# Performance work log

Hardware: AMD Instinct MI355X
Metric: run time of the kernel (lower is better)

The kernel has to match this reference:

```python
import jax, jax.numpy as jnp
import numpy as np

B, V, K, DIN, H, DH, OBS, HID = 2048, 3, 32, 256, 8, 64, 128, 256
REP = H * DH
EPS = 1e-6


def _ln(x, g, b):
    mu = x.mean(-1, keepdims=True)
    var = ((x - mu) ** 2).mean(-1, keepdims=True)
    return (x - mu) * jax.lax.rsqrt(var + 1e-5) * g + b


def setup_inputs() -> dict:
    key = jax.random.key(0)
    ks = iter(jax.random.split(key, 32))
    nrm = lambda shape, s=0.05: jax.random.normal(next(ks), shape, jnp.float32) * s
    return {
        'x_anchor': jax.random.normal(next(ks), (B, V, DIN), jnp.float32),
        'x_neighbors': jax.random.normal(next(ks), (B, V, K, DIN), jnp.float32),
        'edge_weights': jax.random.uniform(next(ks), (B, V, K), jnp.float32),
        'g': jax.random.normal(next(ks), (B, OBS), jnp.float32),
        'aW': nrm((V, DIN, REP)), 'ab': jnp.zeros((V, REP)), 'ag': jnp.ones((V, REP)), 'abeta': jnp.zeros((V, REP)),
        'nW': nrm((V, DIN, REP)), 'nb': jnp.zeros((V, REP)), 'ng': jnp.ones((V, REP)), 'nbeta': jnp.zeros((V, REP)),
        'Wq': nrm((V, H, DH, DH)), 'Wk': nrm((V, H, DH, DH)), 'Wv': nrm((V, H, DH, DH)), 'Wo': nrm((V, H, DH, DH)),
        'geom_log_scale': jnp.zeros((V, H)),
        'cWq': nrm((H, DH, DH)), 'cWk': nrm((H, DH, DH)), 'cWv': nrm((H, DH, DH)), 'cWo': nrm((H, DH, DH)),
        'rW1': nrm((OBS, HID)), 'rb1': jnp.zeros((HID,)),
        'rW2': nrm((HID, HID)), 'rb2': jnp.zeros((HID,)),
        'vW': nrm((HID, H * V)), 'vb': jnp.zeros((H * V,)),
        'mW': nrm((HID, H)), 'mb': jnp.zeros((H,)),
        'gW': nrm((HID, H)), 'gb': jnp.zeros((H,)),
    }


def reference(x_anchor, x_neighbors, edge_weights, g, aW, ab, ag, abeta, nW, nb, ng, nbeta,
              Wq, Wk, Wv, Wo, geom_log_scale, cWq, cWk, cWv, cWo,
              rW1, rb1, rW2, rb2, vW, vb, mW, mb, gW, gb):
    # --- per-view encoders (vectorized over V with a leading v axis) ---
    ha = _ln(jnp.einsum('bvi,vio->bvo', x_anchor, aW) + ab, ag, abeta).reshape(B, V, H, DH)
    hn = _ln(jnp.einsum('bvki,vio->bvko', x_neighbors, nW) + nb[:, None, :],
             ng[:, None, :], nbeta[:, None, :]).reshape(B, V, K, H, DH)
    q = jnp.einsum('bvhd,vhde->bvhe', ha, Wq)
    k = jnp.einsum('bvkhd,vhde->bvkhe', hn, Wk)
    vv = jnp.einsum('bvkhd,vhde->bvkhe', hn, Wv)
    sc = jnp.einsum('bvhd,bvkhd->bvhk', q, k) / np.sqrt(DH).astype(np.float32)
    geom = jax.nn.softplus(geom_log_scale)  # [V,H]
    sc = sc + geom[None, :, :, None] * jnp.log(edge_weights[:, :, None, :] + EPS)
    attn = jax.nn.softmax(sc, axis=-1)
    ho = jnp.einsum('bvhk,bvkhd->bvhd', attn, vv)
    ho = jnp.einsum('bvhd,vhde->bvhe', ho, Wo) + ha  # residual
    view_tokens = jnp.transpose(ho, (0, 2, 1, 3))  # [B,H,V,Dh]
    # --- router ---
    hid = jax.nn.gelu(jnp.dot(g, rW1) + rb1, approximate=False)
    hid = jax.nn.gelu(jnp.dot(hid, rW2) + rb2, approximate=False)
    pi = jax.nn.softmax((jnp.dot(hid, vW) + vb).reshape(B, H, V), axis=-1)
    beta = jax.nn.sigmoid((jnp.dot(hid, mW) + mb)[..., None])  # [B,H,1]
    gate = jax.nn.softmax(jnp.dot(hid, gW) + gb, axis=-1)      # [B,H]
    # --- pi-weighted mixture + cross-view interaction with log-pi prior ---
    mix = jnp.einsum('bhv,bhvd->bhd', pi, view_tokens)
    qc = jnp.einsum('bhd,hde->bhe', mix, cWq)
    kc = jnp.einsum('bhvd,hde->bhve', view_tokens, cWk)
    vc = jnp.einsum('bhvd,hde->bhve', view_tokens, cWv)
    s2 = jnp.einsum('bhd,bhvd->bhv', qc, kc) / np.sqrt(DH).astype(np.float32) + jnp.log(pi + EPS)
    a2 = jax.nn.softmax(s2, axis=-1)
    cr = jnp.einsum('bhv,bhvd->bhd', a2, vc)
    cr = jnp.einsum('bhd,hde->bhe', cr, cWo)
    # mode blend + head gating; head_repr kept unflattened [B,H,Dh]
    return gate[..., None] * (beta * cr + (1.0 - beta) * mix)
```

## Files before the change

kernel.cpp:

```cpp
#include <hip/hip_runtime.h>

#define B_   2048
#define V_   3
#define K_   32
#define DIN_ 256
#define H_   8
#define DH_  64
#define REP_ 512

typedef unsigned short u16;
typedef unsigned int   u32;
typedef __bf16 bf8 __attribute__((ext_vector_type(8)));
typedef float  f4  __attribute__((ext_vector_type(4)));

static __device__ __forceinline__ u16 f2bf(float f) {
  union { float f; u32 i; } x; x.f = f;
  u32 r = (x.i + 0x7FFFu + ((x.i >> 16) & 1u)) >> 16;
  return (u16)r;
}
static __device__ __forceinline__ float bflo(u32 q) {
  union { u32 i; float f; } x; x.i = q << 16; return x.f;
}
static __device__ __forceinline__ float bfhi(u32 q) {
  union { u32 i; float f; } x; x.i = q & 0xffff0000u; return x.f;
}
static __device__ __forceinline__ u32 pk2bf(float lo, float hi) {
  u32 r;
  asm("v_cvt_pk_bf16_f32 %0, %1, %2" : "=v"(r) : "v"(lo), "v"(hi));
  return r;
}

__global__ __launch_bounds__(256) void k0_fuse(
    const float* __restrict__ nW, const float* __restrict__ aW,
    const float* __restrict__ Wv,
    const float* __restrict__ Wq, const float* __restrict__ Wk,
    u16* __restrict__ nWt, u16* __restrict__ aWt, u16* __restrict__ Wvt,
    float* __restrict__ Wqk)
{
  __shared__ float sm8[8192];
  int bid = blockIdx.x, t = threadIdx.x;
  if (bid < 1536) {
    int id = bid * 256 + t;
    int v  = id / 131072, r  = id % 131072;
    int kt = r / 16384,   r2 = r % 16384;
    int n  = r2 >> 5;
    int s  = (r2 >> 3) & 3;
    int m  = r2 & 7;
    int c  = s ^ ((n >> 1) & 3);
    int k  = kt * 32 + c * 8 + m;
    int src = (v * 256 + k) * 512 + n;
    nWt[id] = f2bf(nW[src]);
    aWt[id] = f2bf(aW[src]);
  } else if (bid < 1920) {
    int j = (bid - 1536) * 256 + t;
    int vh = j >> 12, r = j & 4095;
    int e = r >> 6, d = r & 63;
    Wvt[j] = f2bf(Wv[(vh * 64 + d) * 64 + e]);
  } else {
    int vh = bid - 1920;
    float* wq = sm8;
    float* wkT = sm8 + 4096;
    #pragma unroll
    for (int i = 0; i < 16; ++i) {
      int idx = i * 256 + t;
      wq[idx] = Wq[(long)vh * 4096 + idx];
      int e = idx >> 6, c = idx & 63;
      wkT[c * 64 + e] = Wk[(long)vh * 4096 + e * 64 + c];
    }
    __syncthreads();
    int d = t >> 2, e0 = (t & 3) * 16;
    float acc[16];
    #pragma unroll
    for (int j = 0; j < 16; ++j) acc[j] = 0.f;
    for (int c = 0; c < 64; ++c) {
      float a = wq[d * 64 + c];
      const float* wr = &wkT[c * 64 + e0];
      #pragma unroll
      for (int j = 0; j < 16; ++j) acc[j] += a * wr[j];
    }
    #pragma unroll
    for (int j = 0; j < 16; ++j) Wqk[(long)vh * 4096 + d * 64 + e0 + j] = acc[j];
  }
}

__global__ __launch_bounds__(256) void k_tq(
    const float* __restrict__ ha, const float* __restrict__ Wqk,
    float* __restrict__ tB)
{
  __shared__ float hs[512];
  int bv = blockIdx.x, t = threadIdx.x;
  int v = bv % 3;
  hs[t]       = ha[(long)bv * 512 + t];
  hs[256 + t] = ha[(long)bv * 512 + 256 + t];
  __syncthreads();
  int h = t >> 5, e0 = (t & 31) * 2;
  const float* wq = Wqk + ((long)v * 8 + h) * 4096 + e0;
  const float* hv = &hs[h * 64];
  float a0 = 0.f, a1 = 0.f;
  #pragma unroll 4
  for (int d = 0; d < 64; ++d) {
    float x = hv[d];
    float2 wv = *(const float2*)&wq[d * 64];
    a0 += x * wv.x;
    a1 += x * wv.y;
  }
  tB[(long)bv * 512 + h * 64 + e0]     = a0 * 0.125f;
  tB[(long)bv * 512 + h * 64 + e0 + 1] = a1 * 0.125f;
}

__global__ __launch_bounds__(512, 4) void k1a_anchor(
    const float* __restrict__ X,
    const u16*   __restrict__ Wt,
    const float* __restrict__ bias,
    const float* __restrict__ gamma,
    const float* __restrict__ betap,
    float* __restrict__ ha)
{
  __shared__ u16 A[64 * 256];
  __shared__ u16 Bt[16384];
  __shared__ float lnP1[256], lnP2[256], muRs[128];

  const int v = blockIdx.y, blk = blockIdx.x, t = threadIdx.x;
  const int w = t >> 6, l = t & 63, lm = l & 15, lg = l >> 4;
  const int wm = w & 1, wn = w >> 1;

  const u16* Wbase = Wt + (long)v * 131072;

  uint4 pf[4];
  {
    const uint4* gp = (const uint4*)(Wbase + t * 8);
    #pragma unroll
    for (int r = 0; r < 4; ++r) pf[r] = gp[r * 512];
  }

  {
    int row = t >> 3;
    int cbase = (t & 7) * 32;
    int b = blk * 64 + row;
    const float4* src = (const float4*)(X + (long)(b * 3 + v) * 256 + cbase);
    int sw = row & 7;
    #pragma unroll
    for (int j = 0; j < 8; ++j) {
      float4 f = src[j];
      int col = cbase + j * 4;
      int c = col >> 3, m = col & 7;
      uint2 u;
      u.x = pk2bf(f.x, f.y);
      u.y = pk2bf(f.z, f.w);
      *(uint2*)&A[row * 256 + ((c ^ sw) << 3) + m] = u;
    }
  }

  f4 acc[2][8];
  #pragma unroll
  for (int i = 0; i < 2; ++i)
    #pragma unroll
    for (int j = 0; j < 8; ++j) { f4 z = {0.f, 0.f, 0.f, 0.f}; acc[i][j] = z; }

  for (int kt = 0; kt < 8; ++kt) {
    __syncthreads();
    *(uint4*)&Bt[t * 8]         = pf[0];
    *(uint4*)&Bt[t * 8 + 4096]  = pf[1];
    *(uint4*)&Bt[t * 8 + 8192]  = pf[2];
    *(uint4*)&Bt[t * 8 + 12288] = pf[3];
    __syncthreads();
    if (kt < 7) {
      const uint4* gp = (const uint4*)(Wbase + (kt + 1) * 16384 + t * 8);
      #pragma unroll
      for (int r = 0; r < 4; ++r) pf[r] = gp[r * 512];
    }
    bf8 af[2];
    #pragma unroll
    for (int tm = 0; tm < 2; ++tm) {
      int row = wm * 32 + tm * 16 + lm;
      int c = kt * 4 + lg;
      af[tm] = *(const bf8*)&A[row * 256 + ((c ^ (row & 7)) << 3)];
    }
    #pragma unroll
    for (int tn = 0; tn < 8; ++tn) {
      int n = wn * 128 + tn * 16 + lm;
      bf8 bv = *(const bf8*)&Bt[n * 32 + ((lg ^ ((n >> 1) & 3)) << 3)];
      acc[0][tn] = __builtin_amdgcn_mfma_f32_16x16x32_bf16(bv, af[0], acc[0][tn], 0, 0, 0);
      acc[1][tn] = __builtin_amdgcn_mfma_f32_16x16x32_bf16(bv, af[1], acc[1][tn], 0, 0, 0);
    }
  }

  #pragma unroll
  for (int tn = 0; tn < 8; ++tn) {
    float4 bb = *(const float4*)&bias[v * 512 + wn * 128 + tn * 16 + lg * 4];
    #pragma unroll
    for (int r = 0; r < 4; ++r) { acc[0][tn][r] += ((const float*)&bb)[r]; acc[1][tn][r] += ((const float*)&bb)[r]; }
  }

  #pragma unroll
  for (int tm = 0; tm < 2; ++tm) {
    float s1 = 0.f, s2 = 0.f;
    #pragma unroll
    for (int tn = 0; tn < 8; ++tn)
      #pragma unroll
      for (int r = 0; r < 4; ++r) { float z = acc[tm][tn][r]; s1 += z; s2 += z * z; }
    s1 += __shfl_xor(s1, 16, 64); s2 += __shfl_xor(s2, 16, 64);
    s1 += __shfl_xor(s1, 32, 64); s2 += __shfl_xor(s2, 32, 64);
    if (lg == 0) {
      int row = wm * 32 + tm * 16 + lm;
      lnP1[row * 4 + wn] = s1;
      lnP2[row * 4 + wn] = s2;
    }
  }
  __syncthreads();
  if (t < 64) {
    float p = lnP1[t * 4] + lnP1[t * 4 + 1] + lnP1[t * 4 + 2] + lnP1[t * 4 + 3];
    float q = lnP2[t * 4] + lnP2[t * 4 + 1] + lnP2[t * 4 + 2] + lnP2[t * 4 + 3];
    float mu = p * (1.f / 512.f);
    float var = q * (1.f / 512.f) - mu * mu;
    muRs[t]      = mu;
    muRs[64 + t] = rsqrtf(var + 1e-5f);
  }
  __syncthreads();

  {
    float mu0 = muRs[wm * 32 + lm],      rs0 = muRs[64 + wm * 32 + lm];
    float mu1 = muRs[wm * 32 + 16 + lm], rs1 = muRs[64 + wm * 32 + 16 + lm];
    int b0g = blk * 64 + wm * 32 + lm, b1g = b0g + 16;
    #pragma unroll
    for (int tn = 0; tn < 8; ++tn) {
      int col0 = wn * 128 + tn * 16 + lg * 4;
      float4 g4 = *(const float4*)&gamma[v * 512 + col0];
      float4 b4 = *(const float4*)&betap[v * 512 + col0];
      float4 y;
      y.x = (acc[0][tn][0] - mu0) * rs0 * g4.x + b4.x;
      y.y = (acc[0][tn][1] - mu0) * rs0 * g4.y + b4.y;
      y.z = (acc[0][tn][2] - mu0) * rs0 * g4.z + b4.z;
      y.w = (acc[0][tn][3] - mu0) * rs0 * g4.w + b4.w;
      *(float4*)&ha[(long)(b0g * 3 + v) * 512 + col0] = y;
      y.x = (acc[1][tn][0] - mu1) * rs1 * g4.x + b4.x;
      y.y = (acc[1][tn][1] - mu1) * rs1 * g4.y + b4.y;
      y.z = (acc[1][tn][2] - mu1) * rs1 * g4.z + b4.z;
      y.w = (acc[1][tn][3] - mu1) * rs1 * g4.w + b4.w;
      *(float4*)&ha[(long)(b1g * 3 + v) * 512 + col0] = y;
    }
  }
}

union K12Smem {
  struct { u16 A[64 * 256]; u16 Bt[16384]; } p;
  u16 S[64 * 512];
};

__global__ __launch_bounds__(512, 4) void k12_fused(
    const float* __restrict__ X,
    const u16*   __restrict__ Wt,
    const float* __restrict__ bias,
    const float* __restrict__ gamma,
    const float* __restrict__ betap,
    const float* __restrict__ ha,
    const u16*   __restrict__ Wvt,
    const float* __restrict__ tB,
    const float* __restrict__ Wo,
    const float* __restrict__ ew,
    const float* __restrict__ gls,
    float* __restrict__ vt)
{
  __shared__ K12Smem sm;
  __shared__ float tS[1024];
  __shared__ float aS[512];
  __shared__ float oSbuf[1024];
  float* lnP1 = oSbuf;
  float* lnP2 = oSbuf + 256;
  float* muRs = oSbuf + 512;

  const int v = blockIdx.y, blk = blockIdx.x, t = threadIdx.x;
  const int w = t >> 6, l = t & 63, lm = l & 15, lg = l >> 4;
  const int wm = w & 1, wn = w >> 1;

  const u16* Wbase = Wt + (long)v * 131072;

  uint4 pf[4];
  {
    const uint4* gp = (const uint4*)(Wbase + t * 8);
    #pragma unroll
    for (int r = 0; r < 4; ++r) pf[r] = gp[r * 512];
  }

  {
    int row = t >> 3;
    int cbase = (t & 7) * 32;
    int b = blk * 2 + (row >> 5);
    long grow = ((long)(b * 3 + v) * 32 + (row & 31)) * 256;
    const float4* src = (const float4*)(X + grow + cbase);
    int sw = row & 7;
    #pragma unroll
    for (int j = 0; j < 8; ++j) {
      float4 f = src[j];
      int col = cbase + j * 4;
      int c = col >> 3, m = col & 7;
      uint2 u;
      u.x = pk2bf(f.x, f.y);
      u.y = pk2bf(f.z, f.w);
      *(uint2*)&sm.p.A[row * 256 + ((c ^ sw) << 3) + m] = u;
    }
  }
  {
    int b = t >> 8, e = (t & 255) * 2;
    *(float2*)&tS[b * 512 + e] =
        *(const float2*)&tB[((long)(blk * 2 + b) * 3 + v) * 512 + e];
  }

  f4 acc[2][8];
  #pragma unroll
  for (int i = 0; i < 2; ++i)
    #pragma unroll
    for (int j = 0; j < 8; ++j) { f4 z = {0.f, 0.f, 0.f, 0.f}; acc[i][j] = z; }

  for (int kt = 0; kt < 8; ++kt) {
    __syncthreads();
    *(uint4*)&sm.p.Bt[t * 8]         = pf[0];
    *(uint4*)&sm.p.Bt[t * 8 + 4096]  = pf[1];
    *(uint4*)&sm.p.Bt[t * 8 + 8192]  = pf[2];
    *(uint4*)&sm.p.Bt[t * 8 + 12288] = pf[3];
    __syncthreads();
    if (kt < 7) {
      const uint4* gp = (const uint4*)(Wbase + (kt + 1) * 16384 + t * 8);
      #pragma unroll
      for (int r = 0; r < 4; ++r) pf[r] = gp[r * 512];
    }
    bf8 af[2];
    #pragma unroll
    for (int tm = 0; tm < 2; ++tm) {
      int row = wm * 32 + tm * 16 + lm;
      int c = kt * 4 + lg;
      af[tm] = *(const bf8*)&sm.p.A[row * 256 + ((c ^ (row & 7)) << 3)];
    }
    #pragma unroll
    for (int tn = 0; tn < 8; ++tn) {
      int n = wn * 128 + tn * 16 + lm;
      bf8 bv = *(const bf8*)&sm.p.Bt[n * 32 + ((lg ^ ((n >> 1) & 3)) << 3)];
      acc[0][tn] = __builtin_amdgcn_mfma_f32_16x16x32_bf16(bv, af[0], acc[0][tn], 0, 0, 0);
      acc[1][tn] = __builtin_amdgcn_mfma_f32_16x16x32_bf16(bv, af[1], acc[1][tn], 0, 0, 0);
    }
  }

  #pragma unroll
  for (int tn = 0; tn < 8; ++tn) {
    float4 bb = *(const float4*)&bias[v * 512 + wn * 128 + tn * 16 + lg * 4];
    #pragma unroll
    for (int r = 0; r < 4; ++r) { acc[0][tn][r] += ((const float*)&bb)[r]; acc[1][tn][r] += ((const float*)&bb)[r]; }
  }

  #pragma unroll
  for (int tm = 0; tm < 2; ++tm) {
    float s1 = 0.f, s2 = 0.f;
    #pragma unroll
    for (int tn = 0; tn < 8; ++tn)
      #pragma unroll
      for (int r = 0; r < 4; ++r) { float z = acc[tm][tn][r]; s1 += z; s2 += z * z; }
    s1 += __shfl_xor(s1, 16, 64); s2 += __shfl_xor(s2, 16, 64);
    s1 += __shfl_xor(s1, 32, 64); s2 += __shfl_xor(s2, 32, 64);
    if (lg == 0) {
      int row = wm * 32 + tm * 16 + lm;
      lnP1[row * 4 + wn] = s1;
      lnP2[row * 4 + wn] = s2;
    }
  }
  __syncthreads();
  if (t < 64) {
    float p = lnP1[t * 4] + lnP1[t * 4 + 1] + lnP1[t * 4 + 2] + lnP1[t * 4 + 3];
    float q = lnP2[t * 4] + lnP2[t * 4 + 1] + lnP2[t * 4 + 2] + lnP2[t * 4 + 3];
    float mu = p * (1.f / 512.f);
    float var = q * (1.f / 512.f) - mu * mu;
    muRs[t]      = mu;
    muRs[64 + t] = rsqrtf(var + 1e-5f);
  }
  __syncthreads();

  {
    float mu0 = muRs[wm * 32 + lm],      rs0 = muRs[64 + wm * 32 + lm];
    float mu1 = muRs[wm * 32 + 16 + lm], rs1 = muRs[64 + wm * 32 + 16 + lm];
    int row0 = wm * 32 + lm, row1 = row0 + 16;
    int sw0 = row0 & 7, sw1 = row1 & 7;
    #pragma unroll
    for (int tn = 0; tn < 8; ++tn) {
      int col0 = wn * 128 + tn * 16 + lg * 4;
      int c = col0 >> 3, m0 = col0 & 7;
      float4 g4 = *(const float4*)&gamma[v * 512 + col0];
      float4 b4 = *(const float4*)&betap[v * 512 + col0];
      {
        float y0 = (acc[0][tn][0] - mu0) * rs0 * g4.x + b4.x;
        float y1 = (acc[0][tn][1] - mu0) * rs0 * g4.y + b4.y;
        float y2 = (acc[0][tn][2] - mu0) * rs0 * g4.z + b4.z;
        float y3 = (acc[0][tn][3] - mu0) * rs0 * g4.w + b4.w;
        uint2 p;
        p.x = pk2bf(y0, y1);
        p.y = pk2bf(y2, y3);
        *(uint2*)&sm.S[row0 * 512 + ((c ^ sw0) << 3) + m0] = p;
      }
      {
        float y0 = (acc[1][tn][0] - mu1) * rs1 * g4.x + b4.x;
        float y1 = (acc[1][tn][1] - mu1) * rs1 * g4.y + b4.y;
        float y2 = (acc[1][tn][2] - mu1) * rs1 * g4.z + b4.z;
        float y3 = (acc[1][tn][3] - mu1) * rs1 * g4.w + b4.w;
        uint2 p;
        p.x = pk2bf(y0, y1);
        p.y = pk2bf(y2, y3);
        *(uint2*)&sm.S[row1 * 512 + ((c ^ sw1) << 3) + m0] = p;
      }
    }
  }
  __syncthreads();

  {
    int b = t >> 8, h = (t >> 5) & 7, k = t & 31;
    float x = gls[v * 8 + h];
    float gsc = (x > 20.f) ? x : log1pf(expf(x));
    int r = b * 32 + k, sw = r & 7;
    const float* tb = &tS[(b * 8 + h) * 64];
    float s = 0.f;
    #pragma unroll
    for (int j = 0; j < 8; ++j) {
      int c8 = h * 8 + j;
      uint4 q = *(const uint4*)&sm.S[r * 512 + ((c8 ^ sw) << 3)];
      const float* tj = tb + j * 8;
      s += tj[0] * bflo(q.x) + tj[1] * bfhi(q.x)
         + tj[2] * bflo(q.y) + tj[3] * bfhi(q.y)
         + tj[4] * bflo(q.z) + tj[5] * bfhi(q.z)
         + tj[6] * bflo(q.w) + tj[7] * bfhi(q.w);
    }
    float e_w = ew[((long)(blk * 2 + b) * 3 + v) * 32 + k];
    s += gsc * logf(e_w + 1e-6f);
    float m = s;
    #pragma unroll
    for (int d = 1; d < 32; d <<= 1) m = fmaxf(m, __shfl_xor(m, d, 64));
    float exs = expf(s - m), sum = exs;
    #pragma unroll
    for (int d = 1; d < 32; d <<= 1) sum += __shfl_xor(sum, d, 64);
    aS[(b * 8 + h) * 32 + k] = exs / sum;
  }
  __syncthreads();

  #pragma unroll 1
  for (int i = 0; i < 2; ++i) {
    int p = w * 2 + i, b = p >> 3, h = p & 7;
    const u16* wvg = Wvt + (long)(v * 8 + h) * 4096;
    f4 aV[2][4];
    #pragma unroll
    for (int a = 0; a < 2; ++a)
      #pragma unroll
      for (int j = 0; j < 4; ++j) { f4 z = {0.f, 0.f, 0.f, 0.f}; aV[a][j] = z; }
    #pragma unroll
    for (int ks = 0; ks < 2; ++ks) {
      int ko = ks * 32 + lg * 8;
      bf8 af[2];
      #pragma unroll
      for (int tm = 0; tm < 2; ++tm) {
        int r = b * 32 + tm * 16 + lm;
        int c8 = h * 8 + ks * 4 + lg;
        af[tm] = *(const bf8*)&sm.S[r * 512 + ((c8 ^ (r & 7)) << 3)];
      }
      #pragma unroll
      for (int tn = 0; tn < 4; ++tn) {
        bf8 bv = *(const bf8*)&wvg[(tn * 16 + lm) * 64 + ko];
        #pragma unroll
        for (int tm = 0; tm < 2; ++tm)
          aV[tm][tn] = __builtin_amdgcn_mfma_f32_16x16x32_bf16(af[tm], bv, aV[tm][tn], 0, 0, 0);
      }
    }
    float pp[4] = {0.f, 0.f, 0.f, 0.f};
    #pragma unroll
    for (int tm = 0; tm < 2; ++tm)
      #pragma unroll
      for (int r4 = 0; r4 < 4; ++r4) {
        int k = tm * 16 + lg * 4 + r4;
        float a = aS[p * 32 + k];
        #pragma unroll
        for (int tn = 0; tn < 4; ++tn) pp[tn] += a * aV[tm][tn][r4];
      }
    #pragma unroll
    for (int tn = 0; tn < 4; ++tn) {
      float x = pp[tn];
      x += __shfl_xor(x, 16, 64);
      x += __shfl_xor(x, 32, 64);
      if (l < 16) oSbuf[p * 64 + tn * 16 + lm] = x;
    }
  }
  __syncthreads();

  {
    int h = t >> 6, e = t & 63;
    const float* wo = Wo + (long)(v * 8 + h) * 4096;
    float a0 = ha[((long)(blk * 2 + 0) * 3 + v) * 512 + h * 64 + e];
    float a1 = ha[((long)(blk * 2 + 1) * 3 + v) * 512 + h * 64 + e];
    const float* o0 = &oSbuf[h * 64];
    const float* o1 = &oSbuf[512 + h * 64];
    #pragma unroll 8
    for (int d = 0; d < 64; ++d) {
      float wv = wo[d * 64 + e];
      a0 += o0[d] * wv;
      a1 += o1[d] * wv;
    }
    vt[(((long)(blk * 2 + 0) * 8 + h) * 3 + v) * 64 + e] = a0;
    vt[(((long)(blk * 2 + 1) * 8 + h) * 3 + v) * 64 + e] = a1;
  }
}

__global__ __launch_bounds__(256) void k34_router_cross(
    const float* __restrict__ g,
    const float* __restrict__ rW1, const float* __restrict__ rb1,
    const float* __restrict__ rW2, const float* __restrict__ rb2,
    const float* __restrict__ vW, const float* __restrict__ vb,
    const float* __restrict__ mW, const float* __restrict__ mb,
    const float* __restrict__ gW, const float* __restrict__ gb,
    const float* __restrict__ vtg,
    const float* __restrict__ cWq, const float* __restrict__ cWk,
    const float* __restrict__ cWv, const float* __restrict__ cWo,
    float* __restrict__ out)
{
  __shared__ float smem[12544];
  __shared__ float gs[512], h1[1024], h2[1024], lgt[160];
  float* vts   = smem;
  float* mixs  = smem + 6144;
  float* buf1  = smem + 8192;
  float* buf2  = smem + 10240;
  float* a2s   = smem + 12288;
  float* pis   = smem + 12384;
  float* betas = smem + 12480;
  float* gates = smem + 12512;

  int t = threadIdx.x, bb = blockIdx.x * 4;

  {
    const float4* src = (const float4*)(vtg + (long)bb * 1536);
    #pragma unroll
    for (int r = 0; r < 6; ++r) ((float4*)vts)[r * 256 + t] = src[r * 256 + t];
    gs[t]       = g[(long)bb * 128 + t];
    gs[256 + t] = g[(long)bb * 128 + 256 + t];
  }
  __syncthreads();

  {
    int bl = t >> 6, e0 = (t & 63) * 4;
    float acc[4];
    #pragma unroll
    for (int j = 0; j < 4; ++j) acc[j] = rb1[e0 + j];
    for (int i = 0; i < 128; ++i) {
      float gv = gs[bl * 128 + i];
      const float* wr = rW1 + i * 256 + e0;
      #pragma unroll
      for (int j = 0; j < 4; ++j) acc[j] += gv * wr[j];
    }
    #pragma unroll
    for (int j = 0; j < 4; ++j) { float x = acc[j]; h1[bl * 256 + e0 + j] = 0.5f * x * (1.f + erff(x * 0.70710678118f)); }
  }
  __syncthreads();
  {
    int bl = t >> 6, e0 = (t & 63) * 4;
    float acc[4];
    #pragma unroll
    for (int j = 0; j < 4; ++j) acc[j] = rb2[e0 + j];
    for (int i = 0; i < 256; ++i) {
      float hv = h1[bl * 256 + i];
      const float* wr = rW2 + i * 256 + e0;
      #pragma unroll
      for (int j = 0; j < 4; ++j) acc[j] += hv * wr[j];
    }
    #pragma unroll
    for (int j = 0; j < 4; ++j) { float x = acc[j]; h2[bl * 256 + e0 + j] = 0.5f * x * (1.f + erff(x * 0.70710678118f)); }
  }
  __syncthreads();
  if (t < 160) {
    int bl = t / 40, j = t % 40;
    const float* W; float bs; int col, stride;
    if (j < 24)      { W = vW; col = j;      stride = 24; bs = vb[j]; }
    else if (j < 32) { W = mW; col = j - 24; stride = 8;  bs = mb[j - 24]; }
    else             { W = gW; col = j - 32; stride = 8;  bs = gb[j - 32]; }
    float acc = bs;
    for (int i = 0; i < 256; ++i) acc += h2[bl * 256 + i] * W[i * stride + col];
    lgt[bl * 40 + j] = acc;
  }
  __syncthreads();
  if (t < 4) {
    const float* L = &lgt[t * 40];
    #pragma unroll
    for (int hh = 0; hh < 8; ++hh) {
      float a0 = L[hh * 3], a1 = L[hh * 3 + 1], a2v = L[hh * 3 + 2];
      float m = fmaxf(a0, fmaxf(a1, a2v));
      float x0 = expf(a0 - m), x1 = expf(a1 - m), x2 = expf(a2v - m);
      float inv = 1.f / (x0 + x1 + x2);
      pis[t * 24 + hh * 3 + 0] = x0 * inv;
      pis[t * 24 + hh * 3 + 1] = x1 * inv;
      pis[t * 24 + hh * 3 + 2] = x2 * inv;
      betas[t * 8 + hh] = 1.f / (1.f + expf(-L[24 + hh]));
    }
    float m = L[32];
    #pragma unroll
    for (int hh = 1; hh < 8; ++hh) m = fmaxf(m, L[32 + hh]);
    float s = 0.f, ex[8];
    #pragma unroll
    for (int hh = 0; hh < 8; ++hh) { ex[hh] = expf(L[32 + hh] - m); s += ex[hh]; }
    float inv = 1.f / s;
    #pragma unroll
    for (int hh = 0; hh < 8; ++hh) gates[t * 8 + hh] = ex[hh] * inv;
  }
  __syncthreads();

  int bl = t >> 6, hh = (t >> 3) & 7, e0 = (t & 7) * 8;
  const float* vbh = &vts[(bl * 8 + hh) * 192];
  {
    float p0 = pis[bl * 24 + hh * 3], p1 = pis[bl * 24 + hh * 3 + 1], p2 = pis[bl * 24 + hh * 3 + 2];
    #pragma unroll
    for (int j = 0; j < 8; ++j) {
      int e = e0 + j;
      mixs[(bl * 8 + hh) * 64 + e] = p0 * vbh[e] + p1 * vbh[64 + e] + p2 * vbh[128 + e];
    }
  }
  __syncthreads();
  {
    float acc[8] = {0.f,0.f,0.f,0.f,0.f,0.f,0.f,0.f};
    const float* M = &mixs[(bl * 8 + hh) * 64];
    for (int d = 0; d < 64; ++d) {
      float mv = M[d];
      const float* wr = &cWq[(hh * 64 + d) * 64 + e0];
      #pragma unroll
      for (int j = 0; j < 8; ++j) acc[j] += mv * wr[j];
    }
    #pragma unroll
    for (int j = 0; j < 8; ++j) buf1[(bl * 8 + hh) * 64 + e0 + j] = acc[j] * 0.125f;
  }
  __syncthreads();
  {
    const float* Q = &buf1[(bl * 8 + hh) * 64];
    #pragma unroll
    for (int d2 = 0; d2 < 8; ++d2) {
      const float* wr = &cWk[(hh * 64 + e0 + d2) * 64];
      float a = 0.f;
      for (int e = 0; e < 64; ++e) a += wr[e] * Q[e];
      buf2[(bl * 8 + hh) * 64 + e0 + d2] = a;
    }
  }
  __syncthreads();
  if (t < 32) {
    int b2 = t >> 3, h2 = t & 7;
    const float* Wd = &buf2[(b2 * 8 + h2) * 64];
    const float* vb2 = &vts[(b2 * 8 + h2) * 192];
    float s[3];
    #pragma unroll
    for (int v3 = 0; v3 < 3; ++v3) {
      float a = 0.f;
      for (int d = 0; d < 64; ++d) a += Wd[d] * vb2[v3 * 64 + d];
      s[v3] = a + logf(pis[b2 * 24 + h2 * 3 + v3] + 1e-6f);
    }
    float m = fmaxf(s[0], fmaxf(s[1], s[2]));
    float x0 = expf(s[0] - m), x1 = expf(s[1] - m), x2 = expf(s[2] - m);
    float inv = 1.f / (x0 + x1 + x2);
    a2s[(b2 * 8 + h2) * 3 + 0] = x0 * inv;
    a2s[(b2 * 8 + h2) * 3 + 1] = x1 * inv;
    a2s[(b2 * 8 + h2) * 3 + 2] = x2 * inv;
  }
  __syncthreads();
  {
    float a0 = a2s[(bl * 8 + hh) * 3], a1 = a2s[(bl * 8 + hh) * 3 + 1], a2v = a2s[(bl * 8 + hh) * 3 + 2];
    #pragma unroll
    for (int j = 0; j < 8; ++j) {
      int e = e0 + j;
      buf1[(bl * 8 + hh) * 64 + e] = a0 * vbh[e] + a1 * vbh[64 + e] + a2v * vbh[128 + e];
    }
  }
  __syncthreads();
  {
    float acc[8] = {0.f,0.f,0.f,0.f,0.f,0.f,0.f,0.f};
    const float* Y = &buf1[(bl * 8 + hh) * 64];
    for (int d = 0; d < 64; ++d) {
      float yv = Y[d];
      const float* wr = &cWv[(hh * 64 + d) * 64 + e0];
      #pragma unroll
      for (int j = 0; j < 8; ++j) acc[j] += yv * wr[j];
    }
    #pragma unroll
    for (int j = 0; j < 8; ++j) buf2[(bl * 8 + hh) * 64 + e0 + j] = acc[j];
  }
  __syncthreads();
  {
    float acc[8] = {0.f,0.f,0.f,0.f,0.f,0.f,0.f,0.f};
    const float* C2 = &buf2[(bl * 8 + hh) * 64];
    for (int d = 0; d < 64; ++d) {
      float cv = C2[d];
      const float* wr = &cWo[(hh * 64 + d) * 64 + e0];
      #pragma unroll
      for (int j = 0; j < 8; ++j) acc[j] += cv * wr[j];
    }
    float bt = betas[bl * 8 + hh], gt = gates[bl * 8 + hh];
    const float* M = &mixs[(bl * 8 + hh) * 64];
    #pragma unroll
    for (int j = 0; j < 8; ++j)
      out[((long)(bb + bl) * 8 + hh) * 64 + e0 + j] = gt * (bt * acc[j] + (1.f - bt) * M[e0 + j]);
  }
}

extern "C" void kernel_launch(void* const* d_in, const int* in_sizes, int n_in,
                              void* d_out, int out_size, void* d_ws, size_t ws_size,
                              hipStream_t stream) {
  const float* x_anchor    = (const float*)d_in[0];
  const float* x_neighbors = (const float*)d_in[1];
  const float* edge_w      = (const float*)d_in[2];
  const float* g           = (const float*)d_in[3];
  const float* aW  = (const float*)d_in[4];
  const float* ab  = (const float*)d_in[5];
  const float* ag  = (const float*)d_in[6];
  const float* abeta = (const float*)d_in[7];
  const float* nW  = (const float*)d_in[8];
  const float* nb  = (const float*)d_in[9];
  const float* ng  = (const float*)d_in[10];
  const float* nbeta = (const float*)d_in[11];
  const float* Wq  = (const float*)d_in[12];
  const float* Wk  = (const float*)d_in[13];
  const float* Wv  = (const float*)d_in[14];
  const float* Wo  = (const float*)d_in[15];
  const float* gls = (const float*)d_in[16];
  const float* cWq = (const float*)d_in[17];
  const float* cWk = (const float*)d_in[18];
  const float* cWv = (const float*)d_in[19];
  const float* cWo = (const float*)d_in[20];
  const float* rW1 = (const float*)d_in[21];
  const float* rb1 = (const float*)d_in[22];
  const float* rW2 = (const float*)d_in[23];
  const float* rb2 = (const float*)d_in[24];
  const float* vW  = (const float*)d_in[25];
  const float* vb  = (const float*)d_in[26];
  const float* mW  = (const float*)d_in[27];
  const float* mb  = (const float*)d_in[28];
  const float* gW  = (const float*)d_in[29];
  const float* gb  = (const float*)d_in[30];

  char* p = (char*)d_ws;
  u16* nWt = (u16*)p;  p += 786432;
  u16* aWt = (u16*)p;  p += 786432;
  u16* Wvt = (u16*)p;  p += 196608;
  float* WqkB = (float*)p; p += 393216;
  float* ha   = (float*)p; p += 12582912;
  float* vtb  = (float*)p; p += 12582912;
  float* tqB  = (float*)p; p += 12582912;
  (void)ws_size;

  k0_fuse<<<1944, 256, 0, stream>>>(nW, aW, Wv, Wq, Wk, nWt, aWt, Wvt, WqkB);
  k1a_anchor<<<dim3(32, 3), 512, 0, stream>>>(x_anchor, aWt, ab, ag, abeta, ha);
  k_tq<<<6144, 256, 0, stream>>>(ha, WqkB, tqB);
  k12_fused<<<dim3(1024, 3), 512, 0, stream>>>(x_neighbors, nWt, nb, ng, nbeta,
                                               ha, Wvt, tqB, Wo, edge_w, gls, vtb);
  k34_router_cross<<<512, 256, 0, stream>>>(g, rW1, rb1, rW2, rb2, vW, vb,
                                            mW, mb, gW, gb, vtb,
                                            cWq, cWk, cWv, cWo, (float*)d_out);
}
```

Baseline: 900.4 us.

## Use direct global-to-LDS weight loads and double-buffer B in 1024-thread k12

Weight tiles are now loaded with global_load_lds straight into shared memory instead of staging through registers. In k1a the fill happens after a barrier each k-step. k12_fused gets a double-buffered B tile so the next tile's load overlaps the current MFMAs. k12 is also widened from 512 to 1024 threads, with each wave owning one 16-row M tile and one attention head, which cuts registers per thread and raises parallelism but increases LDS use per block (extra B buffer plus separate LN scratch) and may reduce resident blocks. Correctness relies on the barrier placement, and there is no explicit wait for the asynchronous LDS loads.

```diff
diff --git a/kernel.cpp b/kernel.cpp
--- a/kernel.cpp
+++ b/kernel.cpp
@@ -28,6 +28,12 @@
   u32 r;
   asm("v_cvt_pk_bf16_f32 %0, %1, %2" : "=v"(r) : "v"(lo), "v"(hi));
   return r;
+}
+
+static __device__ __forceinline__ void gl2lds16(const u16* g, u16* l) {
+  __builtin_amdgcn_global_load_lds(
+      (const __attribute__((address_space(1))) unsigned int*)(g),
+      (__attribute__((address_space(3))) unsigned int*)(l), 16, 0, 0);
 }
 
 __global__ __launch_bounds__(256) void k0_fuse(
@@ -126,11 +132,11 @@
 
   const u16* Wbase = Wt + (long)v * 131072;
 
-  uint4 pf[4];
-  {
-    const uint4* gp = (const uint4*)(Wbase + t * 8);
-    #pragma unroll
-    for (int r = 0; r < 4; ++r) pf[r] = gp[r * 512];
+  {
+    const u16* gp = Wbase + t * 8;
+    u16* lp = &Bt[t * 8];
+    #pragma unroll
+    for (int r = 0; r < 4; ++r) gl2lds16(gp + r * 4096, lp + r * 4096);
   }
 
   {
@@ -158,17 +164,14 @@
     for (int j = 0; j < 8; ++j) { f4 z = {0.f, 0.f, 0.f, 0.f}; acc[i][j] = z; }
 
   for (int kt = 0; kt < 8; ++kt) {
+    if (kt) {
+      __syncthreads();
+      const u16* gp = Wbase + kt * 16384 + t * 8;
+      u16* lp = &Bt[t * 8];
+      #pragma unroll
+      for (int r = 0; r < 4; ++r) gl2lds16(gp + r * 4096, lp + r * 4096);
+    }
     __syncthreads();
-    *(uint4*)&Bt[t * 8]         = pf[0];
-    *(uint4*)&Bt[t * 8 + 4096]  = pf[1];
-    *(uint4*)&Bt[t * 8 + 8192]  = pf[2];
-    *(uint4*)&Bt[t * 8 + 12288] = pf[3];
-    __syncthreads();
-    if (kt < 7) {
-      const uint4* gp = (const uint4*)(Wbase + (kt + 1) * 16384 + t * 8);
-      #pragma unroll
-      for (int r = 0; r < 4; ++r) pf[r] = gp[r * 512];
-    }
     bf8 af[2];
     #pragma unroll
     for (int tm = 0; tm < 2; ++tm) {
@@ -243,11 +246,11 @@
 }
 
 union K12Smem {
-  struct { u16 A[64 * 256]; u16 Bt[16384]; } p;
+  struct { u16 A[64 * 256]; u16 Bt[2][16384]; } p;
   u16 S[64 * 512];
 };
 
-__global__ __launch_bounds__(512, 4) void k12_fused(
+__global__ __launch_bounds__(1024, 4) void k12_fused(
     const float* __restrict__ X,
     const u16*   __restrict__ Wt,
     const float* __restrict__ bias,
@@ -265,34 +268,32 @@
   __shared__ float tS[1024];
   __shared__ float aS[512];
   __shared__ float oSbuf[1024];
-  float* lnP1 = oSbuf;
-  float* lnP2 = oSbuf + 256;
-  float* muRs = oSbuf + 512;
+  __shared__ float lnP1[256], lnP2[256], muRs[128];
 
   const int v = blockIdx.y, blk = blockIdx.x, t = threadIdx.x;
   const int w = t >> 6, l = t & 63, lm = l & 15, lg = l >> 4;
-  const int wm = w & 1, wn = w >> 1;
+  const int wm = w & 3, wn = w >> 2;
 
   const u16* Wbase = Wt + (long)v * 131072;
 
-  uint4 pf[4];
-  {
-    const uint4* gp = (const uint4*)(Wbase + t * 8);
-    #pragma unroll
-    for (int r = 0; r < 4; ++r) pf[r] = gp[r * 512];
-  }
-
-  {
-    int row = t >> 3;
-    int cbase = (t & 7) * 32;
+  {
+    const u16* gp = Wbase + t * 8;
+    u16* lp = &sm.p.Bt[0][t * 8];
+    gl2lds16(gp, lp);
+    gl2lds16(gp + 8192, lp + 8192);
+  }
+
+  {
+    int row = t >> 4;
+    int cq = (t & 15) * 4;
     int b = blk * 2 + (row >> 5);
     long grow = ((long)(b * 3 + v) * 32 + (row & 31)) * 256;
-    const float4* src = (const float4*)(X + grow + cbase);
+    const float* src = X + grow;
     int sw = row & 7;
     #pragma unroll
-    for (int j = 0; j < 8; ++j) {
-      float4 f = src[j];
-      int col = cbase + j * 4;
+    for (int j = 0; j < 4; ++j) {
+      int col = cq + j * 64;
+      float4 f = *(const float4*)(src + col);
       int c = col >> 3, m = col & 7;
       uint2 u;
       u.x = pk2bf(f.x, f.y);
@@ -301,42 +302,32 @@
     }
   }
   {
-    int b = t >> 8, e = (t & 255) * 2;
-    *(float2*)&tS[b * 512 + e] =
-        *(const float2*)&tB[((long)(blk * 2 + b) * 3 + v) * 512 + e];
-  }
-
-  f4 acc[2][8];
+    int b = t >> 9, e = t & 511;
+    tS[t] = tB[((long)(blk * 2 + b) * 3 + v) * 512 + e];
+  }
+
+  f4 acc[8];
   #pragma unroll
-  for (int i = 0; i < 2; ++i)
-    #pragma unroll
-    for (int j = 0; j < 8; ++j) { f4 z = {0.f, 0.f, 0.f, 0.f}; acc[i][j] = z; }
-
+  for (int j = 0; j < 8; ++j) { f4 z = {0.f, 0.f, 0.f, 0.f}; acc[j] = z; }
+
+  const int rowA = wm * 16 + lm;
+  const int swA = rowA & 7;
   for (int kt = 0; kt < 8; ++kt) {
     __syncthreads();
-    *(uint4*)&sm.p.Bt[t * 8]         = pf[0];
-    *(uint4*)&sm.p.Bt[t * 8 + 4096]  = pf[1];
-    *(uint4*)&sm.p.Bt[t * 8 + 8192]  = pf[2];
-    *(uint4*)&sm.p.Bt[t * 8 + 12288] = pf[3];
-    __syncthreads();
     if (kt < 7) {
-      const uint4* gp = (const uint4*)(Wbase + (kt + 1) * 16384 + t * 8);
-      #pragma unroll
-      for (int r = 0; r < 4; ++r) pf[r] = gp[r * 512];
-    }
-    bf8 af[2];
-    #pragma unroll
-    for (int tm = 0; tm < 2; ++tm) {
-      int row = wm * 32 + tm * 16 + lm;
-      int c = kt * 4 + lg;
-      af[tm] = *(const bf8*)&sm.p.A[row * 256 + ((c ^ (row & 7)) << 3)];
-    }
+      const u16* gp = Wbase + (kt + 1) * 16384 + t * 8;
+      u16* lp = &sm.p.Bt[(kt + 1) & 1][t * 8];
+      gl2lds16(gp, lp);
+      gl2lds16(gp + 8192, lp + 8192);
+    }
+    int c = kt * 4 + lg;
+    bf8 af = *(const bf8*)&sm.p.A[rowA * 256 + ((c ^ swA) << 3)];
+    const u16* Bcur = sm.p.Bt[kt & 1];
     #pragma unroll
     for (int tn = 0; tn < 8; ++tn) {
       int n = wn * 128 + tn * 16 + lm;
-      bf8 bv = *(const bf8*)&sm.p.Bt[n * 32 + ((lg ^ ((n >> 1) & 3)) << 3)];
-      acc[0][tn] = __builtin_amdgcn_mfma_f32_16x16x32_bf16(bv, af[0], acc[0][tn], 0, 0, 0);
-      acc[1][tn] = __builtin_amdgcn_mfma_f32_16x16x32_bf16(bv, af[1], acc[1][tn], 0, 0, 0);
+      bf8 bv = *(const bf8*)&Bcur[n * 32 + ((lg ^ ((n >> 1) & 3)) << 3)];
+      acc[tn] = __builtin_amdgcn_mfma_f32_16x16x32_bf16(bv, af, acc[tn], 0, 0, 0);
     }
   }
 
@@ -344,22 +335,20 @@
   for (int tn = 0; tn < 8; ++tn) {
     float4 bb = *(const float4*)&bias[v * 512 + wn * 128 + tn * 16 + lg * 4];
     #pragma unroll
-    for (int r = 0; r < 4; ++r) { acc[0][tn][r] += ((const float*)&bb)[r]; acc[1][tn][r] += ((const float*)&bb)[r]; }
-  }
-
-  #pragma unroll
-  for (int tm = 0; tm < 2; ++tm) {
+    for (int r = 0; r < 4; ++r) acc[tn][r] += ((const float*)&bb)[r];
+  }
+
+  {
     float s1 = 0.f, s2 = 0.f;
     #pragma unroll
     for (int tn = 0; tn < 8; ++tn)
       #pragma unroll
-      for (int r = 0; r < 4; ++r) { float z = acc[tm][tn][r]; s1 += z; s2 += z * z; }
+      for (int r = 0; r < 4; ++r) { float z = acc[tn][r]; s1 += z; s2 += z * z; }
     s1 += __shfl_xor(s1, 16, 64); s2 += __shfl_xor(s2, 16, 64);
     s1 += __shfl_xor(s1, 32, 64); s2 += __shfl_xor(s2, 32, 64);
     if (lg == 0) {
-      int row = wm * 32 + tm * 16 + lm;
-      lnP1[row * 4 + wn] = s1;
-      lnP2[row * 4 + wn] = s2;
+      lnP1[rowA * 4 + wn] = s1;
+      lnP2[rowA * 4 + wn] = s2;
     }
   }
   __syncthreads();
@@ -374,41 +363,26 @@
   __syncthreads();
 
   {
-    float mu0 = muRs[wm * 32 + lm],      rs0 = muRs[64 + wm * 32 + lm];
-    float mu1 = muRs[wm * 32 + 16 + lm], rs1 = muRs[64 + wm * 32 + 16 + lm];
-    int row0 = wm * 32 + lm, row1 = row0 + 16;
-    int sw0 = row0 & 7, sw1 = row1 & 7;
+    float mu0 = muRs[rowA], rs0 = muRs[64 + rowA];
     #pragma unroll
     for (int tn = 0; tn < 8; ++tn) {
       int col0 = wn * 128 + tn * 16 + lg * 4;
       int c = col0 >> 3, m0 = col0 & 7;
       float4 g4 = *(const float4*)&gamma[v * 512 + col0];
       float4 b4 = *(const float4*)&betap[v * 512 + col0];
-      {
-        float y0 = (acc[0][tn][0] - mu0) * rs0 * g4.x + b4.x;
-        float y1 = (acc[0][tn][1] - mu0) * rs0 * g4.y + b4.y;
-        float y2 = (acc[0][tn][2] - mu0) * rs0 * g4.z + b4.z;
-        float y3 = (acc[0][tn][3] - mu0) * rs0 * g4.w + b4.w;
-        uint2 p;
-        p.x = pk2bf(y0, y1);
-        p.y = pk2bf(y2, y3);
-        *(uint2*)&sm.S[row0 * 512 + ((c ^ sw0) << 3) + m0] = p;
-      }
-      {
-        float y0 = (acc[1][tn][0] - mu1) * rs1 * g4.x + b4.x;
-        float y1 = (acc[1][tn][1] - mu1) * rs1 * g4.y + b4.y;
-        float y2 = (acc[1][tn][2] - mu1) * rs1 * g4.z + b4.z;
-        float y3 = (acc[1][tn][3] - mu1) * rs1 * g4.w + b4.w;
-        uint2 p;
-        p.x = pk2bf(y0, y1);
-        p.y = pk2bf(y2, y3);
-        *(uint2*)&sm.S[row1 * 512 + ((c ^ sw1) << 3) + m0] = p;
-      }
-    }
-  }
-  __syncthreads();
-
-  {
+      float y0 = (acc[tn][0] - mu0) * rs0 * g4.x + b4.x;
+      float y1 = (acc[tn][1] - mu0) * rs0 * g4.y + b4.y;
+      float y2 = (acc[tn][2] - mu0) * rs0 * g4.z + b4.z;
+      float y3 = (acc[tn][3] - mu0) * rs0 * g4.w + b4.w;
+      uint2 p;
+      p.x = pk2bf(y0, y1);
+      p.y = pk2bf(y2, y3);
+      *(uint2*)&sm.S[rowA * 512 + ((c ^ swA) << 3) + m0] = p;
+    }
+  }
+  __syncthreads();
+
+  if (t < 512) {
     int b = t >> 8, h = (t >> 5) & 7, k = t & 31;
     float x = gls[v * 8 + h];
     float gsc = (x > 20.f) ? x : log1pf(expf(x));
@@ -437,10 +411,9 @@
   }
   __syncthreads();
 
-  #pragma unroll 1
-  for (int i = 0; i < 2; ++i) {
-    int p = w * 2 + i, b = p >> 3, h = p & 7;
-    const u16* wvg = Wvt + (long)(v * 8 + h) * 4096;
+  {
+    int p = w, b = w >> 3, h = w & 7;
+    const u16* wvg = Wvt + ((long)v * 8 + h) * 4096;
     f4 aV[2][4];
     #pragma unroll
     for (int a = 0; a < 2; ++a)
@@ -449,19 +422,19 @@
     #pragma unroll
     for (int ks = 0; ks < 2; ++ks) {
       int ko = ks * 32 + lg * 8;
-      bf8 af[2];
+      bf8 af2[2];
       #pragma unroll
       for (int tm = 0; tm < 2; ++tm) {
         int r = b * 32 + tm * 16 + lm;
         int c8 = h * 8 + ks * 4 + lg;
-        af[tm] = *(const bf8*)&sm.S[r * 512 + ((c8 ^ (r & 7)) << 3)];
+        af2[tm] = *(const bf8*)&sm.S[r * 512 + ((c8 ^ (r & 7)) << 3)];
       }
       #pragma unroll
       for (int tn = 0; tn < 4; ++tn) {
         bf8 bv = *(const bf8*)&wvg[(tn * 16 + lm) * 64 + ko];
         #pragma unroll
         for (int tm = 0; tm < 2; ++tm)
-          aV[tm][tn] = __builtin_amdgcn_mfma_f32_16x16x32_bf16(af[tm], bv, aV[tm][tn], 0, 0, 0);
+          aV[tm][tn] = __builtin_amdgcn_mfma_f32_16x16x32_bf16(af2[tm], bv, aV[tm][tn], 0, 0, 0);
       }
     }
     float pp[4] = {0.f, 0.f, 0.f, 0.f};
@@ -485,20 +458,13 @@
   __syncthreads();
 
   {
-    int h = t >> 6, e = t & 63;
-    const float* wo = Wo + (long)(v * 8 + h) * 4096;
-    float a0 = ha[((long)(blk * 2 + 0) * 3 + v) * 512 + h * 64 + e];
-    float a1 = ha[((long)(blk * 2 + 1) * 3 + v) * 512 + h * 64 + e];
-    const float* o0 = &oSbuf[h * 64];
-    const float* o1 = &oSbuf[512 + h * 64];
+    int b = t >> 9, h = (t >> 6) & 7, e = t & 63;
+    const float* wo = Wo + ((long)v * 8 + h) * 4096;
+    float a = ha[((long)(blk * 2 + b) * 3 + v) * 512 + h * 64 + e];
+    const float* o = &oSbuf[(b * 8 + h) * 64];
     #pragma unroll 8
-    for (int d = 0; d < 64; ++d) {
-      float wv = wo[d * 64 + e];
-      a0 += o0[d] * wv;
-      a1 += o1[d] * wv;
-    }
-    vt[(((long)(blk * 2 + 0) * 8 + h) * 3 + v) * 64 + e] = a0;
-    vt[(((long)(blk * 2 + 1) * 8 + h) * 3 + v) * 64 + e] = a1;
+    for (int d = 0; d < 64; ++d) a += o[d] * wo[d * 64 + e];
+    vt[(((long)(blk * 2 + b) * 8 + h) * 3 + v) * 64 + e] = a;
   }
 }
 
@@ -743,8 +709,8 @@
   k0_fuse<<<1944, 256, 0, stream>>>(nW, aW, Wv, Wq, Wk, nWt, aWt, Wvt, WqkB);
   k1a_anchor<<<dim3(32, 3), 512, 0, stream>>>(x_anchor, aWt, ab, ag, abeta, ha);
   k_tq<<<6144, 256, 0, stream>>>(ha, WqkB, tqB);
-  k12_fused<<<dim3(1024, 3), 512, 0, stream>>>(x_neighbors, nWt, nb, ng, nbeta,
-                                               ha, Wvt, tqB, Wo, edge_w, gls, vtb);
+  k12_fused<<<dim3(1024, 3), 1024, 0, stream>>>(x_neighbors, nWt, nb, ng, nbeta,
+                                                ha, Wvt, tqB, Wo, edge_w, gls, vtb);
   k34_router_cross<<<512, 256, 0, stream>>>(g, rW1, rb1, rW2, rb2, vW, vb,
                                             mW, mb, gW, gb, vtb,
                                             cWq, cWk, cWv, cWo, (float*)d_out);
```

Result: faster. 784.0 us (-12.9%).

## Fold Wo into Wv weights and stage B tiles via global_load_lds

Applied to the files above, without the earlier changes.

Precomputes Wv·Wo per view and head in the weight-prep kernel, so the attention output lands directly in output space. This removes the per-block Wo matmul epilogue, its shared buffer and a barrier in the fused neighbor kernel. Separately, the B-tile loads in both GEMM kernels switch from register prefetch plus LDS store to direct global-to-LDS loads. That drops register staging, but the next tile is no longer prefetched during compute, so load latency is exposed each k-step.

```diff
diff --git a/kernel.cpp b/kernel.cpp
--- a/kernel.cpp
+++ b/kernel.cpp
@@ -30,11 +30,17 @@
   return r;
 }
 
+static __device__ __forceinline__ void gl2lds16(const u16* g, u16* l) {
+  __builtin_amdgcn_global_load_lds(
+      (const __attribute__((address_space(1))) unsigned int*)(g),
+      (__attribute__((address_space(3))) unsigned int*)(l), 16, 0, 0);
+}
+
 __global__ __launch_bounds__(256) void k0_fuse(
     const float* __restrict__ nW, const float* __restrict__ aW,
-    const float* __restrict__ Wv,
+    const float* __restrict__ Wv, const float* __restrict__ Wo,
     const float* __restrict__ Wq, const float* __restrict__ Wk,
-    u16* __restrict__ nWt, u16* __restrict__ aWt, u16* __restrict__ Wvt,
+    u16* __restrict__ nWt, u16* __restrict__ aWt, u16* __restrict__ Wvot,
     float* __restrict__ Wqk)
 {
   __shared__ float sm8[8192];
@@ -51,13 +57,8 @@
     int src = (v * 256 + k) * 512 + n;
     nWt[id] = f2bf(nW[src]);
     aWt[id] = f2bf(aW[src]);
-  } else if (bid < 1920) {
-    int j = (bid - 1536) * 256 + t;
-    int vh = j >> 12, r = j & 4095;
-    int e = r >> 6, d = r & 63;
-    Wvt[j] = f2bf(Wv[(vh * 64 + d) * 64 + e]);
-  } else {
-    int vh = bid - 1920;
+  } else if (bid < 1560) {
+    int vh = bid - 1536;
     float* wq = sm8;
     float* wkT = sm8 + 4096;
     #pragma unroll
@@ -80,6 +81,30 @@
     }
     #pragma unroll
     for (int j = 0; j < 16; ++j) Wqk[(long)vh * 4096 + d * 64 + e0 + j] = acc[j];
+  } else {
+    int vh = bid - 1560;
+    float* wv = sm8;
+    float* wo = sm8 + 4096;
+    #pragma unroll
+    for (int i = 0; i < 16; ++i) {
+      int idx = i * 256 + t;
+      wv[idx] = Wv[(long)vh * 4096 + idx];
+      wo[idx] = Wo[(long)vh * 4096 + idx];
+    }
+    __syncthreads();
+    int d = t >> 2, e0 = (t & 3) * 16;
+    float acc[16];
+    #pragma unroll
+    for (int j = 0; j < 16; ++j) acc[j] = 0.f;
+    for (int c = 0; c < 64; ++c) {
+      float a = wv[d * 64 + c];
+      const float* wr = &wo[c * 64 + e0];
+      #pragma unroll
+      for (int j = 0; j < 16; ++j) acc[j] += a * wr[j];
+    }
+    #pragma unroll
+    for (int j = 0; j < 16; ++j)
+      Wvot[((long)vh * 64 + e0 + j) * 64 + d] = f2bf(acc[j]);
   }
 }
 
@@ -126,11 +151,11 @@
 
   const u16* Wbase = Wt + (long)v * 131072;
 
-  uint4 pf[4];
-  {
-    const uint4* gp = (const uint4*)(Wbase + t * 8);
-    #pragma unroll
-    for (int r = 0; r < 4; ++r) pf[r] = gp[r * 512];
+  {
+    const u16* gp = Wbase + t * 8;
+    u16* lp = &Bt[t * 8];
+    #pragma unroll
+    for (int r = 0; r < 4; ++r) gl2lds16(gp + r * 4096, lp + r * 4096);
   }
 
   {
@@ -158,17 +183,14 @@
     for (int j = 0; j < 8; ++j) { f4 z = {0.f, 0.f, 0.f, 0.f}; acc[i][j] = z; }
 
   for (int kt = 0; kt < 8; ++kt) {
+    if (kt) {
+      __syncthreads();
+      const u16* gp = Wbase + kt * 16384 + t * 8;
+      u16* lp = &Bt[t * 8];
+      #pragma unroll
+      for (int r = 0; r < 4; ++r) gl2lds16(gp + r * 4096, lp + r * 4096);
+    }
     __syncthreads();
-    *(uint4*)&Bt[t * 8]         = pf[0];
-    *(uint4*)&Bt[t * 8 + 4096]  = pf[1];
-    *(uint4*)&Bt[t * 8 + 8192]  = pf[2];
-    *(uint4*)&Bt[t * 8 + 12288] = pf[3];
-    __syncthreads();
-    if (kt < 7) {
-      const uint4* gp = (const uint4*)(Wbase + (kt + 1) * 16384 + t * 8);
-      #pragma unroll
-      for (int r = 0; r < 4; ++r) pf[r] = gp[r * 512];
-    }
     bf8 af[2];
     #pragma unroll
     for (int tm = 0; tm < 2; ++tm) {
@@ -254,9 +276,8 @@
     const float* __restrict__ gamma,
     const float* __restrict__ betap,
     const float* __restrict__ ha,
-    const u16*   __restrict__ Wvt,
+    const u16*   __restrict__ Wvot,
     const float* __restrict__ tB,
-    const float* __restrict__ Wo,
     const float* __restrict__ ew,
     const float* __restrict__ gls,
     float* __restrict__ vt)
@@ -264,10 +285,7 @@
   __shared__ K12Smem sm;
   __shared__ float tS[1024];
   __shared__ float aS[512];
-  __shared__ float oSbuf[1024];
-  float* lnP1 = oSbuf;
-  float* lnP2 = oSbuf + 256;
-  float* muRs = oSbuf + 512;
+  __shared__ float lnP1[256], lnP2[256], muRs[128];
 
   const int v = blockIdx.y, blk = blockIdx.x, t = threadIdx.x;
   const int w = t >> 6, l = t & 63, lm = l & 15, lg = l >> 4;
@@ -275,11 +293,11 @@
 
   const u16* Wbase = Wt + (long)v * 131072;
 
-  uint4 pf[4];
-  {
-    const uint4* gp = (const uint4*)(Wbase + t * 8);
-    #pragma unroll
-    for (int r = 0; r < 4; ++r) pf[r] = gp[r * 512];
+  {
+    const u16* gp = Wbase + t * 8;
+    u16* lp = &sm.p.Bt[t * 8];
+    #pragma unroll
+    for (int r = 0; r < 4; ++r) gl2lds16(gp + r * 4096, lp + r * 4096);
   }
 
   {
@@ -313,17 +331,14 @@
     for (int j = 0; j < 8; ++j) { f4 z = {0.f, 0.f, 0.f, 0.f}; acc[i][j] = z; }
 
   for (int kt = 0; kt < 8; ++kt) {
+    if (kt) {
+      __syncthreads();
+      const u16* gp = Wbase + kt * 16384 + t * 8;
+      u16* lp = &sm.p.Bt[t * 8];
+      #pragma unroll
+      for (int r = 0; r < 4; ++r) gl2lds16(gp + r * 4096, lp + r * 4096);
+    }
     __syncthreads();
-    *(uint4*)&sm.p.Bt[t * 8]         = pf[0];
-    *(uint4*)&sm.p.Bt[t * 8 + 4096]  = pf[1];
-    *(uint4*)&sm.p.Bt[t * 8 + 8192]  = pf[2];
-    *(uint4*)&sm.p.Bt[t * 8 + 12288] = pf[3];
-    __syncthreads();
-    if (kt < 7) {
-      const uint4* gp = (const uint4*)(Wbase + (kt + 1) * 16384 + t * 8);
-      #pragma unroll
-      for (int r = 0; r < 4; ++r) pf[r] = gp[r * 512];
-    }
     bf8 af[2];
     #pragma unroll
     for (int tm = 0; tm < 2; ++tm) {
@@ -440,7 +455,7 @@
   #pragma unroll 1
   for (int i = 0; i < 2; ++i) {
     int p = w * 2 + i, b = p >> 3, h = p & 7;
-    const u16* wvg = Wvt + (long)(v * 8 + h) * 4096;
+    const u16* wvg = Wvot + ((long)v * 8 + h) * 4096;
     f4 aV[2][4];
     #pragma unroll
     for (int a = 0; a < 2; ++a)
@@ -449,19 +464,19 @@
     #pragma unroll
     for (int ks = 0; ks < 2; ++ks) {
       int ko = ks * 32 + lg * 8;
-      bf8 af[2];
+      bf8 af2[2];
       #pragma unroll
       for (int tm = 0; tm < 2; ++tm) {
         int r = b * 32 + tm * 16 + lm;
         int c8 = h * 8 + ks * 4 + lg;
-        af[tm] = *(const bf8*)&sm.S[r * 512 + ((c8 ^ (r & 7)) << 3)];
+        af2[tm] = *(const bf8*)&sm.S[r * 512 + ((c8 ^ (r & 7)) << 3)];
       }
       #pragma unroll
       for (int tn = 0; tn < 4; ++tn) {
         bf8 bv = *(const bf8*)&wvg[(tn * 16 + lm) * 64 + ko];
         #pragma unroll
         for (int tm = 0; tm < 2; ++tm)
-          aV[tm][tn] = __builtin_amdgcn_mfma_f32_16x16x32_bf16(af[tm], bv, aV[tm][tn], 0, 0, 0);
+          aV[tm][tn] = __builtin_amdgcn_mfma_f32_16x16x32_bf16(af2[tm], bv, aV[tm][tn], 0, 0, 0);
       }
     }
     float pp[4] = {0.f, 0.f, 0.f, 0.f};
@@ -474,31 +489,17 @@
         #pragma unroll
         for (int tn = 0; tn < 4; ++tn) pp[tn] += a * aV[tm][tn][r4];
       }
+    int bg = blk * 2 + b;
     #pragma unroll
     for (int tn = 0; tn < 4; ++tn) {
       float x = pp[tn];
       x += __shfl_xor(x, 16, 64);
       x += __shfl_xor(x, 32, 64);
-      if (l < 16) oSbuf[p * 64 + tn * 16 + lm] = x;
-    }
-  }
-  __syncthreads();
-
-  {
-    int h = t >> 6, e = t & 63;
-    const float* wo = Wo + (long)(v * 8 + h) * 4096;
-    float a0 = ha[((long)(blk * 2 + 0) * 3 + v) * 512 + h * 64 + e];
-    float a1 = ha[((long)(blk * 2 + 1) * 3 + v) * 512 + h * 64 + e];
-    const float* o0 = &oSbuf[h * 64];
-    const float* o1 = &oSbuf[512 + h * 64];
-    #pragma unroll 8
-    for (int d = 0; d < 64; ++d) {
-      float wv = wo[d * 64 + e];
-      a0 += o0[d] * wv;
-      a1 += o1[d] * wv;
-    }
-    vt[(((long)(blk * 2 + 0) * 8 + h) * 3 + v) * 64 + e] = a0;
-    vt[(((long)(blk * 2 + 1) * 8 + h) * 3 + v) * 64 + e] = a1;
+      if (l < 16) {
+        float hav = ha[((long)bg * 3 + v) * 512 + h * 64 + tn * 16 + lm];
+        vt[(((long)bg * 8 + h) * 3 + v) * 64 + tn * 16 + lm] = x + hav;
+      }
+    }
   }
 }
 
@@ -733,18 +734,18 @@
   char* p = (char*)d_ws;
   u16* nWt = (u16*)p;  p += 786432;
   u16* aWt = (u16*)p;  p += 786432;
-  u16* Wvt = (u16*)p;  p += 196608;
+  u16* Wvot = (u16*)p; p += 196608;
   float* WqkB = (float*)p; p += 393216;
   float* ha   = (float*)p; p += 12582912;
   float* vtb  = (float*)p; p += 12582912;
   float* tqB  = (float*)p; p += 12582912;
   (void)ws_size;
 
-  k0_fuse<<<1944, 256, 0, stream>>>(nW, aW, Wv, Wq, Wk, nWt, aWt, Wvt, WqkB);
+  k0_fuse<<<1584, 256, 0, stream>>>(nW, aW, Wv, Wo, Wq, Wk, nWt, aWt, Wvot, WqkB);
   k1a_anchor<<<dim3(32, 3), 512, 0, stream>>>(x_anchor, aWt, ab, ag, abeta, ha);
   k_tq<<<6144, 256, 0, stream>>>(ha, WqkB, tqB);
   k12_fused<<<dim3(1024, 3), 512, 0, stream>>>(x_neighbors, nWt, nb, ng, nbeta,
-                                               ha, Wvt, tqB, Wo, edge_w, gls, vtb);
+                                               ha, Wvot, tqB, edge_w, gls, vtb);
   k34_router_cross<<<512, 256, 0, stream>>>(g, rW1, rb1, rW2, rb2, vW, vb,
                                             mW, mb, gW, gb, vtb,
                                             cWq, cWk, cWv, cWo, (float*)d_out);
```

Measured after the change: 739.7 us. 17.8% less time.
